# Kernel tuning notes

Measured on AMD Instinct MI355X. Metric: run time of the kernel, lower is better.

## Reference

```python
import jax, jax.numpy as jnp
import numpy as np

B, T_FRAMES, C, WS = 8, 8, 32, 128
N = 1024            # sample_size^2 points per frame
HW = WS * WS        # 16384 grid cells
BT = B * T_FRAMES


def setup_inputs() -> dict:
    key = jax.random.key(0)
    k1, k2, k3 = jax.random.split(key, 3)
    rng = np.random.default_rng(0)
    # per-frame grid-cell id for each of N points
    pose = rng.integers(0, HW, size=(BT, N))
    sorted_indices = np.argsort(pose, axis=1).astype(np.int32)
    sorted_pose = np.take_along_axis(pose, sorted_indices, axis=1)
    seq_unique_list = np.zeros((BT, N), dtype=np.int32)
    seq_unique_counts = np.zeros((BT, N), dtype=np.int32)
    for i in range(BT):
        u, c = np.unique(sorted_pose[i], return_counts=True)
        seq_unique_list[i, : len(u)] = u
        seq_unique_counts[i, : len(u)] = c
    return {
        "w_part": jax.random.normal(k1, (BT, N, C), dtype=jnp.float32),
        "sorted_indices": jnp.asarray(sorted_indices),
        "seq_unique_list": jnp.asarray(seq_unique_list),
        "seq_unique_counts": jnp.asarray(seq_unique_counts),
        "past_w": jax.random.normal(k2, (B, C, WS, WS), dtype=jnp.float32),
        "past_w_num_mask": jax.random.uniform(k3, (B, 1, WS, WS), dtype=jnp.float32) * 4.0,
        "T": T_FRAMES,
    }


def reference(w_part, sorted_indices, seq_unique_list, seq_unique_counts, past_w, past_w_num_mask, T):
    bt, n, c = w_part.shape
    b = bt // T
    ws = past_w.shape[2]
    hw = ws * ws
    # F.normalize(dim=-1), eps=1e-12
    wp = w_part / jnp.maximum(jnp.linalg.norm(w_part, axis=-1, keepdims=True), 1e-12)
    # gather: reorder points so same-cell points are contiguous
    gathered = jnp.take_along_axis(wp, sorted_indices[..., None].astype(jnp.int32), axis=1)  # (bt, n, c)
    counts = seq_unique_counts  # (bt, n) padded with zeros
    # segment id of each point from cumulative counts (points are sorted by cell)
    cum = jnp.cumsum(counts, axis=1)
    pt = jnp.arange(n)
    seg = jax.vmap(lambda cu: jnp.searchsorted(cu, pt, side='right'))(cum)  # (bt, n)
    sums = jax.vmap(lambda g, s: jax.ops.segment_sum(g, s, num_segments=n))(gathered, seg)  # (bt, n, c)
    means = sums / jnp.maximum(counts, 1)[..., None].astype(wp.dtype)
    # scatter means into dense grid; padded (count==0) slots routed out-of-bounds and dropped
    idx = jnp.where(counts > 0, seq_unique_list, hw)
    scat = jax.vmap(lambda m, i: jnp.zeros((hw, c), wp.dtype).at[i].set(m, mode='drop'))(means, idx)  # (bt, hw, c)
    mask = jax.vmap(lambda ct, i: jnp.zeros((hw,), wp.dtype).at[i].set(ct.astype(wp.dtype), mode='drop'))(counts, idx)
    new_w = scat.reshape(b, T, hw, c).mean(axis=1)                 # (b, hw, c)
    new_w = new_w.transpose(0, 2, 1).reshape(b, c, ws, ws)          # (b, c, ws, ws)
    w_num_mask = mask.reshape(b, T, hw).sum(axis=1).reshape(b, 1, ws, ws)
    # merge with past map; denominator is detached in the original
    new_w_num_mask = jax.lax.stop_gradient(w_num_mask) + jax.lax.stop_gradient(past_w_num_mask)
    new_w_num_mask = jnp.where(new_w_num_mask == 0, 1.0, new_w_num_mask)
    w = (new_w * w_num_mask + past_w * past_w_num_mask) / new_w_num_mask
    return w, new_w_num_mask
```

## Files before the change

### kernel.cpp

```cpp
#include <hip/hip_runtime.h>
#include <climits>

#define BATCH   8
#define TFRAMES 8
#define BT      (BATCH * TFRAMES)
#define NPTS    1024
#define NCH     32
#define WS      128
#define HW      (WS * WS)
#define CELLS   64
#define CHUNKS  (HW / CELLS)
#define CPAD    33
#define TPB     256

__global__ __launch_bounds__(256) void scan_kernel(
    const int* __restrict__ uniq_cnt,
    const int* __restrict__ uniq_list,
    int4*      __restrict__ entries,
    int*       __restrict__ ranges)
{
    __shared__ int s_key[NPTS];
    __shared__ int s_wsum[4];

    const int tid  = threadIdx.x;
    const int bt   = blockIdx.x;
    const int wave = tid >> 6;
    const int lane = tid & 63;

    const int4 c4 = reinterpret_cast<const int4*>(uniq_cnt + bt * NPTS)[tid];
    const int4 l4 = reinterpret_cast<const int4*>(uniq_list + bt * NPTS)[tid];
    s_key[tid * 4 + 0] = (c4.x > 0) ? l4.x : INT_MAX;
    s_key[tid * 4 + 1] = (c4.y > 0) ? l4.y : INT_MAX;
    s_key[tid * 4 + 2] = (c4.z > 0) ? l4.z : INT_MAX;
    s_key[tid * 4 + 3] = (c4.w > 0) ? l4.w : INT_MAX;

    const int lsum = c4.x + c4.y + c4.z + c4.w;

    int inc = lsum;
#pragma unroll
    for (int d = 1; d < 64; d <<= 1) {
        const int v = __shfl_up(inc, d);
        if (lane >= d) inc += v;
    }
    if (lane == 63) s_wsum[wave] = inc;
    __syncthreads();

    int woff = 0;
#pragma unroll
    for (int w = 0; w < 4; ++w)
        if (w < wave) woff += s_wsum[w];

    int st = woff + inc - lsum;
    int4* ep = entries + (size_t)bt * NPTS + tid * 4;
    ep[0] = make_int4(l4.x, c4.x, st, 0);             st += c4.x;
    ep[1] = make_int4(l4.y, c4.y, st, 0);             st += c4.y;
    ep[2] = make_int4(l4.z, c4.z, st, 0);             st += c4.z;
    ep[3] = make_int4(l4.w, c4.w, st, 0);

    for (int k = tid; k <= CHUNKS; k += 256) {
        const int X = k * CELLS;
        int lo = 0, hi = NPTS;
        while (lo < hi) {
            const int mid = (lo + hi) >> 1;
            if (s_key[mid] < X) lo = mid + 1; else hi = mid;
        }
        ranges[bt * (CHUNKS + 1) + k] = lo;
    }
}

__global__ __launch_bounds__(TPB, 8) void tile_kernel(
    const float* __restrict__ w_part,
    const int*   __restrict__ sorted_idx,
    const int4*  __restrict__ entries,
    const int*   __restrict__ ranges,
    const float* __restrict__ past_w,
    const float* __restrict__ past_mask,
    float*       __restrict__ out_w,
    float*       __restrict__ out_mask)
{
    __shared__ float s_acc[CELLS][CPAD];
    __shared__ float s_mask[CELLS];

    const int tid   = threadIdx.x;
    const int b     = blockIdx.x & (BATCH - 1);
    const int chunk = blockIdx.x >> 3;
    const int cb    = chunk * CELLS;

    const int cellq = tid & 15;
    const int cgrp  = tid >> 4;
    const int c0    = cgrp * 2;
    const int gc    = cb + cellq * 4;
    const size_t mbase = (size_t)b * HW + gc;
    const float4 pm4 = *reinterpret_cast<const float4*>(past_mask + mbase);
    const size_t a0 = ((size_t)b * NCH + c0) * HW + gc;
    const float4 pw0 = *reinterpret_cast<const float4*>(past_w + a0);
    const float4 pw1 = *reinterpret_cast<const float4*>(past_w + a0 + HW);

    float* flat = &s_acc[0][0];
    for (int i = tid; i < CELLS * CPAD; i += TPB) flat[i] = 0.0f;
    if (tid < CELLS) s_mask[tid] = 0.0f;
    __syncthreads();

    const int wave  = tid >> 6;
    const int lane  = tid & 63;
    const int slot  = lane >> 3;
    const int lane8 = lane & 7;

#pragma unroll
    for (int tt = 0; tt < 2; ++tt) {
        const int t  = wave * 2 + tt;
        const int bt = b * TFRAMES + t;
        const int lo = ranges[bt * (CHUNKS + 1) + chunk];
        const int hi = ranges[bt * (CHUNKS + 1) + chunk + 1];
        const int4* __restrict__ ent = entries + (size_t)bt * NPTS;
        const int*  __restrict__ si  = sorted_idx + bt * NPTS;
        const float* __restrict__ wp = w_part + (size_t)bt * NPTS * NCH;

        for (int e = lo + slot; e < hi; e += 8) {
            const int4 meta = ent[e];
            const int cell  = meta.x;
            const int cnt   = meta.y;
            const int start = meta.z;
            float4 lacc = make_float4(0.f, 0.f, 0.f, 0.f);
            for (int p = start; p < start + cnt; ++p) {
                const int j = si[p];
                const float4 v = *reinterpret_cast<const float4*>(
                    wp + (size_t)j * NCH + lane8 * 4);
                float ss = v.x * v.x + v.y * v.y + v.z * v.z + v.w * v.w;
                ss += __shfl_xor(ss, 1);
                ss += __shfl_xor(ss, 2);
                ss += __shfl_xor(ss, 4);
                const float scale = 1.0f / fmaxf(sqrtf(ss), 1e-12f);
                lacc.x += v.x * scale;
                lacc.y += v.y * scale;
                lacc.z += v.z * scale;
                lacc.w += v.w * scale;
            }
            const float invc = 1.0f / (float)cnt;
            const int cl = cell - cb;
            float* ap = &s_acc[cl][lane8 * 4];
            atomicAdd(ap + 0, lacc.x * invc);
            atomicAdd(ap + 1, lacc.y * invc);
            atomicAdd(ap + 2, lacc.z * invc);
            atomicAdd(ap + 3, lacc.w * invc);
            if (lane8 == 0) atomicAdd(&s_mask[cl], (float)cnt);
        }
    }
    __syncthreads();

    const float invT = 1.0f / (float)TFRAMES;
    float m[4], pm[4], r[4], dn[4];
    pm[0] = pm4.x; pm[1] = pm4.y; pm[2] = pm4.z; pm[3] = pm4.w;
#pragma unroll
    for (int i = 0; i < 4; ++i) {
        m[i] = s_mask[cellq * 4 + i];
        const float nwm = m[i] + pm[i];
        dn[i] = (nwm == 0.0f) ? 1.0f : nwm;
        r[i] = 1.0f / dn[i];
    }
    if (cgrp == 0) {
        *reinterpret_cast<float4*>(out_mask + mbase) =
            make_float4(dn[0], dn[1], dn[2], dn[3]);
    }

    float4 o0, o1;
    o0.x = (s_acc[cellq * 4 + 0][c0] * invT * m[0] + pw0.x * pm[0]) * r[0];
    o0.y = (s_acc[cellq * 4 + 1][c0] * invT * m[1] + pw0.y * pm[1]) * r[1];
    o0.z = (s_acc[cellq * 4 + 2][c0] * invT * m[2] + pw0.z * pm[2]) * r[2];
    o0.w = (s_acc[cellq * 4 + 3][c0] * invT * m[3] + pw0.w * pm[3]) * r[3];
    o1.x = (s_acc[cellq * 4 + 0][c0 + 1] * invT * m[0] + pw1.x * pm[0]) * r[0];
    o1.y = (s_acc[cellq * 4 + 1][c0 + 1] * invT * m[1] + pw1.y * pm[1]) * r[1];
    o1.z = (s_acc[cellq * 4 + 2][c0 + 1] * invT * m[2] + pw1.z * pm[2]) * r[2];
    o1.w = (s_acc[cellq * 4 + 3][c0 + 1] * invT * m[3] + pw1.w * pm[3]) * r[3];
    *reinterpret_cast<float4*>(out_w + a0)      = o0;
    *reinterpret_cast<float4*>(out_w + a0 + HW) = o1;
}

extern "C" void kernel_launch(void* const* d_in, const int* in_sizes, int n_in,
                              void* d_out, int out_size, void* d_ws, size_t ws_size,
                              hipStream_t stream) {
    (void)in_sizes; (void)n_in; (void)out_size; (void)ws_size;

    const float* w_part     = (const float*)d_in[0];
    const int*   sorted_idx = (const int*)d_in[1];
    const int*   uniq_list  = (const int*)d_in[2];
    const int*   uniq_cnt   = (const int*)d_in[3];
    const float* past_w     = (const float*)d_in[4];
    const float* past_mask  = (const float*)d_in[5];

    float* out      = (float*)d_out;
    float* out_w    = out;
    float* out_mask = out + (size_t)BATCH * NCH * HW;

    int4* entries = (int4*)d_ws;
    int*  ranges  = (int*)(entries + (size_t)BT * NPTS);

    scan_kernel<<<BT, 256, 0, stream>>>(uniq_cnt, uniq_list, entries, ranges);

    tile_kernel<<<BATCH * CHUNKS, TPB, 0, stream>>>(
        w_part, sorted_idx, entries, ranges,
        past_w, past_mask, out_w, out_mask);
}
```

Baseline: 29.86 us.

## Split segment-mean computation into separate point-parallel kernel before tile scatter

Adds a per-point segment-id map in the scan kernel and a new means_kernel that normalizes points in parallel and accumulates per-segment means via shared atomics, writing them to a workspace buffer. The tile kernel then reads precomputed means instead of looping serially over points per segment. This removes the variable-length inner loop and load imbalance from the tile kernel, at the cost of a memset, an extra kernel launch and a global round-trip of the means buffer.

```diff
diff --git a/kernel.cpp b/kernel.cpp
--- a/kernel.cpp
+++ b/kernel.cpp
@@ -17,9 +17,11 @@
     const int* __restrict__ uniq_cnt,
     const int* __restrict__ uniq_list,
     int4*      __restrict__ entries,
-    int*       __restrict__ ranges)
+    int*       __restrict__ ranges,
+    int*       __restrict__ segof)
 {
     __shared__ int s_key[NPTS];
+    __shared__ int s_segof[NPTS];
     __shared__ int s_wsum[4];
 
     const int tid  = threadIdx.x;
@@ -51,11 +53,25 @@
         if (w < wave) woff += s_wsum[w];
 
     int st = woff + inc - lsum;
-    int4* ep = entries + (size_t)bt * NPTS + tid * 4;
-    ep[0] = make_int4(l4.x, c4.x, st, 0);             st += c4.x;
-    ep[1] = make_int4(l4.y, c4.y, st, 0);             st += c4.y;
-    ep[2] = make_int4(l4.z, c4.z, st, 0);             st += c4.z;
+    const int e_base = tid * 4;
+    int4* ep = entries + (size_t)bt * NPTS + e_base;
+
+    ep[0] = make_int4(l4.x, c4.x, st, 0);
+    for (int q = 0; q < c4.x; ++q) s_segof[st + q] = e_base + 0;
+    st += c4.x;
+    ep[1] = make_int4(l4.y, c4.y, st, 0);
+    for (int q = 0; q < c4.y; ++q) s_segof[st + q] = e_base + 1;
+    st += c4.y;
+    ep[2] = make_int4(l4.z, c4.z, st, 0);
+    for (int q = 0; q < c4.z; ++q) s_segof[st + q] = e_base + 2;
+    st += c4.z;
     ep[3] = make_int4(l4.w, c4.w, st, 0);
+    for (int q = 0; q < c4.w; ++q) s_segof[st + q] = e_base + 3;
+
+    __syncthreads();
+
+    reinterpret_cast<int4*>(segof + bt * NPTS)[tid] =
+        *reinterpret_cast<int4*>(&s_segof[tid * 4]);
 
     for (int k = tid; k <= CHUNKS; k += 256) {
         const int X = k * CELLS;
@@ -68,9 +84,71 @@
     }
 }
 
-__global__ __launch_bounds__(TPB, 8) void tile_kernel(
+__global__ __launch_bounds__(256) void means_kernel(
     const float* __restrict__ w_part,
     const int*   __restrict__ sorted_idx,
+    const int*   __restrict__ segof,
+    const int4*  __restrict__ entries,
+    float*       __restrict__ means)
+{
+    __shared__ float s_seg[257][CPAD];
+
+    const int tid = threadIdx.x;
+    const int bt  = blockIdx.x >> 2;
+    const int p0  = (blockIdx.x & 3) * 256;
+
+    const int* __restrict__ sgo = segof + bt * NPTS;
+    const int s0 = sgo[p0];
+    const int s1 = sgo[p0 + 255];
+    const int nseg = s1 - s0 + 1;
+
+    float* flat = &s_seg[0][0];
+    for (int i = tid; i < nseg * CPAD; i += 256) flat[i] = 0.0f;
+    __syncthreads();
+
+    const int pt    = tid >> 3;
+    const int lane8 = tid & 7;
+    const int* __restrict__ si = sorted_idx + bt * NPTS;
+    const float* __restrict__ wp = w_part + (size_t)bt * NPTS * NCH;
+
+#pragma unroll
+    for (int pass = 0; pass < 8; ++pass) {
+        const int p = p0 + pass * 32 + pt;
+        const int j = si[p];
+        const float4 v = *reinterpret_cast<const float4*>(
+            wp + (size_t)j * NCH + lane8 * 4);
+        float ss = v.x * v.x + v.y * v.y + v.z * v.z + v.w * v.w;
+        ss += __shfl_xor(ss, 1);
+        ss += __shfl_xor(ss, 2);
+        ss += __shfl_xor(ss, 4);
+        const float scale = 1.0f / fmaxf(sqrtf(ss), 1e-12f);
+        const int ls = sgo[p] - s0;
+        float* ap = &s_seg[ls][lane8 * 4];
+        atomicAdd(ap + 0, v.x * scale);
+        atomicAdd(ap + 1, v.y * scale);
+        atomicAdd(ap + 2, v.z * scale);
+        atomicAdd(ap + 3, v.w * scale);
+    }
+    __syncthreads();
+
+    const int grp = tid >> 5;
+    const int ch  = tid & 31;
+    const int4* __restrict__ ent = entries + (size_t)bt * NPTS;
+    for (int le = grp; le < nseg; le += 8) {
+        const int e = s0 + le;
+        const int4 meta = ent[e];
+        const int cnt   = meta.y;
+        const int start = meta.z;
+        const float val = s_seg[le][ch] * (1.0f / (float)cnt);
+        float* dst = means + ((size_t)bt * NPTS + e) * NCH + ch;
+        const bool owned = (start >= p0) && (start + cnt <= p0 + 256);
+        if (owned) *dst = val;
+        else       atomicAdd(dst, val);
+    }
+}
+
+__global__ __launch_bounds__(TPB, 8) void tile_kernel(
+    const float* __restrict__ means,
     const int4*  __restrict__ entries,
     const int*   __restrict__ ranges,
     const float* __restrict__ past_w,
@@ -112,38 +190,20 @@
         const int bt = b * TFRAMES + t;
         const int lo = ranges[bt * (CHUNKS + 1) + chunk];
         const int hi = ranges[bt * (CHUNKS + 1) + chunk + 1];
-        const int4* __restrict__ ent = entries + (size_t)bt * NPTS;
-        const int*  __restrict__ si  = sorted_idx + bt * NPTS;
-        const float* __restrict__ wp = w_part + (size_t)bt * NPTS * NCH;
+        const int4*  __restrict__ ent = entries + (size_t)bt * NPTS;
+        const float* __restrict__ mns = means + (size_t)bt * NPTS * NCH;
 
         for (int e = lo + slot; e < hi; e += 8) {
             const int4 meta = ent[e];
-            const int cell  = meta.x;
-            const int cnt   = meta.y;
-            const int start = meta.z;
-            float4 lacc = make_float4(0.f, 0.f, 0.f, 0.f);
-            for (int p = start; p < start + cnt; ++p) {
-                const int j = si[p];
-                const float4 v = *reinterpret_cast<const float4*>(
-                    wp + (size_t)j * NCH + lane8 * 4);
-                float ss = v.x * v.x + v.y * v.y + v.z * v.z + v.w * v.w;
-                ss += __shfl_xor(ss, 1);
-                ss += __shfl_xor(ss, 2);
-                ss += __shfl_xor(ss, 4);
-                const float scale = 1.0f / fmaxf(sqrtf(ss), 1e-12f);
-                lacc.x += v.x * scale;
-                lacc.y += v.y * scale;
-                lacc.z += v.z * scale;
-                lacc.w += v.w * scale;
-            }
-            const float invc = 1.0f / (float)cnt;
-            const int cl = cell - cb;
+            const float4 mv = *reinterpret_cast<const float4*>(
+                mns + (size_t)e * NCH + lane8 * 4);
+            const int cl = meta.x - cb;
             float* ap = &s_acc[cl][lane8 * 4];
-            atomicAdd(ap + 0, lacc.x * invc);
-            atomicAdd(ap + 1, lacc.y * invc);
-            atomicAdd(ap + 2, lacc.z * invc);
-            atomicAdd(ap + 3, lacc.w * invc);
-            if (lane8 == 0) atomicAdd(&s_mask[cl], (float)cnt);
+            atomicAdd(ap + 0, mv.x);
+            atomicAdd(ap + 1, mv.y);
+            atomicAdd(ap + 2, mv.z);
+            atomicAdd(ap + 3, mv.w);
+            if (lane8 == 0) atomicAdd(&s_mask[cl], (float)meta.y);
         }
     }
     __syncthreads();
@@ -192,12 +252,17 @@
     float* out_w    = out;
     float* out_mask = out + (size_t)BATCH * NCH * HW;
 
-    int4* entries = (int4*)d_ws;
-    int*  ranges  = (int*)(entries + (size_t)BT * NPTS);
-
-    scan_kernel<<<BT, 256, 0, stream>>>(uniq_cnt, uniq_list, entries, ranges);
+    int4*  entries = (int4*)d_ws;
+    int*   ranges  = (int*)(entries + (size_t)BT * NPTS);
+    int*   segof   = ranges + (size_t)BT * (CHUNKS + 1);
+    float* means   = (float*)(segof + (size_t)BT * NPTS);
+
+    hipMemsetAsync(means, 0, (size_t)BT * NPTS * NCH * sizeof(float), stream);
+
+    scan_kernel<<<BT, 256, 0, stream>>>(uniq_cnt, uniq_list, entries, ranges, segof);
+
+    means_kernel<<<BT * 4, 256, 0, stream>>>(w_part, sorted_idx, segof, entries, means);
 
     tile_kernel<<<BATCH * CHUNKS, TPB, 0, stream>>>(
-        w_part, sorted_idx, entries, ranges,
-        past_w, past_mask, out_w, out_mask);
-}
+        means, entries, ranges, past_w, past_mask, out_w, out_mask);
+}
```

Result: slower. 62.73 us (+110.0%).

## Prefetch first point indices into entries and widen tiles to 128 cells

Applied to the files above, without the earlier changes.

The scan kernel now stores the first two sorted point indices of each cell directly in the entry record, packing the cell id and count together. It also writes (lo,hi) ranges as int2 pairs. The tile kernel doubles cells per block and threads per block, giving one wave per frame. It issues the metadata and first feature loads before zeroing shared memory, which shortens the dependent-load chain (entry, sorted index, feature). In exchange the scan kernel does extra gathers, and packing the count into the upper 16 bits assumes cell ids below 65536.

```diff
diff --git a/kernel.cpp b/kernel.cpp
--- a/kernel.cpp
+++ b/kernel.cpp
@@ -8,19 +8,21 @@
 #define NCH     32
 #define WS      128
 #define HW      (WS * WS)
-#define CELLS   64
+#define CELLS   128
 #define CHUNKS  (HW / CELLS)
 #define CPAD    33
-#define TPB     256
+#define TPB     512
 
 __global__ __launch_bounds__(256) void scan_kernel(
     const int* __restrict__ uniq_cnt,
     const int* __restrict__ uniq_list,
+    const int* __restrict__ sorted_idx,
     int4*      __restrict__ entries,
-    int*       __restrict__ ranges)
+    int2*      __restrict__ ranges2)
 {
     __shared__ int s_key[NPTS];
     __shared__ int s_wsum[4];
+    __shared__ int s_bnd[CHUNKS + 1];
 
     const int tid  = threadIdx.x;
     const int bt   = blockIdx.x;
@@ -50,29 +52,40 @@
     for (int w = 0; w < 4; ++w)
         if (w < wave) woff += s_wsum[w];
 
+    const int* __restrict__ si = sorted_idx + bt * NPTS;
     int st = woff + inc - lsum;
     int4* ep = entries + (size_t)bt * NPTS + tid * 4;
-    ep[0] = make_int4(l4.x, c4.x, st, 0);             st += c4.x;
-    ep[1] = make_int4(l4.y, c4.y, st, 0);             st += c4.y;
-    ep[2] = make_int4(l4.z, c4.z, st, 0);             st += c4.z;
-    ep[3] = make_int4(l4.w, c4.w, st, 0);
-
-    for (int k = tid; k <= CHUNKS; k += 256) {
-        const int X = k * CELLS;
+
+    const int cc[4] = {c4.x, c4.y, c4.z, c4.w};
+    const int ll[4] = {l4.x, l4.y, l4.z, l4.w};
+#pragma unroll
+    for (int k = 0; k < 4; ++k) {
+        const int cnt = cc[k];
+        const int j0  = (cnt > 0) ? si[st]     : 0;
+        const int j1  = (cnt > 1) ? si[st + 1] : 0;
+        ep[k] = make_int4(ll[k] | (cnt << 16), j0, j1, st);
+        st += cnt;
+    }
+
+    if (tid <= CHUNKS) {
+        const int X = tid * CELLS;
         int lo = 0, hi = NPTS;
         while (lo < hi) {
             const int mid = (lo + hi) >> 1;
             if (s_key[mid] < X) lo = mid + 1; else hi = mid;
         }
-        ranges[bt * (CHUNKS + 1) + k] = lo;
-    }
+        s_bnd[tid] = lo;
+    }
+    __syncthreads();
+    if (tid < CHUNKS)
+        ranges2[bt * CHUNKS + tid] = make_int2(s_bnd[tid], s_bnd[tid + 1]);
 }
 
 __global__ __launch_bounds__(TPB, 8) void tile_kernel(
     const float* __restrict__ w_part,
     const int*   __restrict__ sorted_idx,
     const int4*  __restrict__ entries,
-    const int*   __restrict__ ranges,
+    const int2*  __restrict__ ranges2,
     const float* __restrict__ past_w,
     const float* __restrict__ past_mask,
     float*       __restrict__ out_w,
@@ -86,8 +99,8 @@
     const int chunk = blockIdx.x >> 3;
     const int cb    = chunk * CELLS;
 
-    const int cellq = tid & 15;
-    const int cgrp  = tid >> 4;
+    const int cellq = tid & 31;
+    const int cgrp  = tid >> 5;
     const int c0    = cgrp * 2;
     const int gc    = cb + cellq * 4;
     const size_t mbase = (size_t)b * HW + gc;
@@ -96,55 +109,84 @@
     const float4 pw0 = *reinterpret_cast<const float4*>(past_w + a0);
     const float4 pw1 = *reinterpret_cast<const float4*>(past_w + a0 + HW);
 
-    float* flat = &s_acc[0][0];
-    for (int i = tid; i < CELLS * CPAD; i += TPB) flat[i] = 0.0f;
-    if (tid < CELLS) s_mask[tid] = 0.0f;
-    __syncthreads();
-
     const int wave  = tid >> 6;
     const int lane  = tid & 63;
     const int slot  = lane >> 3;
     const int lane8 = lane & 7;
 
-#pragma unroll
-    for (int tt = 0; tt < 2; ++tt) {
-        const int t  = wave * 2 + tt;
-        const int bt = b * TFRAMES + t;
-        const int lo = ranges[bt * (CHUNKS + 1) + chunk];
-        const int hi = ranges[bt * (CHUNKS + 1) + chunk + 1];
-        const int4* __restrict__ ent = entries + (size_t)bt * NPTS;
-        const int*  __restrict__ si  = sorted_idx + bt * NPTS;
-        const float* __restrict__ wp = w_part + (size_t)bt * NPTS * NCH;
-
-        for (int e = lo + slot; e < hi; e += 8) {
-            const int4 meta = ent[e];
-            const int cell  = meta.x;
-            const int cnt   = meta.y;
-            const int start = meta.z;
-            float4 lacc = make_float4(0.f, 0.f, 0.f, 0.f);
-            for (int p = start; p < start + cnt; ++p) {
+    const int bt = b * TFRAMES + wave;
+    const int2 rg = ranges2[bt * CHUNKS + chunk];
+    const int lo = rg.x, hi = rg.y;
+
+    const int4* __restrict__ ent = entries + (size_t)bt * NPTS;
+    const float* __restrict__ wp = w_part + (size_t)bt * NPTS * NCH;
+
+    const int eA = lo + slot;
+    const int eB = eA + 8;
+    const bool vA = (eA < hi);
+    const bool vB = (eB < hi);
+    const int4 metaA = ent[vA ? eA : 0];
+    const int4 metaB = ent[vB ? eB : 0];
+    const float4 vwA = *reinterpret_cast<const float4*>(
+        wp + (size_t)metaA.y * NCH + lane8 * 4);
+    const float4 vwB = *reinterpret_cast<const float4*>(
+        wp + (size_t)metaB.y * NCH + lane8 * 4);
+
+    float* flat = &s_acc[0][0];
+    for (int i = tid; i < CELLS * CPAD; i += TPB) flat[i] = 0.0f;
+    if (tid < CELLS) s_mask[tid] = 0.0f;
+    __syncthreads();
+
+    const int* __restrict__ si = sorted_idx + bt * NPTS;
+    auto process = [&](const int4 meta, const float4 v0) {
+        const int cell  = meta.x & 0xFFFF;
+        const int cnt   = meta.x >> 16;
+        float ss = v0.x * v0.x + v0.y * v0.y + v0.z * v0.z + v0.w * v0.w;
+        ss += __shfl_xor(ss, 1);
+        ss += __shfl_xor(ss, 2);
+        ss += __shfl_xor(ss, 4);
+        const float s0 = 1.0f / fmaxf(sqrtf(ss), 1e-12f);
+        float4 lacc = make_float4(v0.x * s0, v0.y * s0, v0.z * s0, v0.w * s0);
+        if (cnt > 1) {
+            const float4 v1 = *reinterpret_cast<const float4*>(
+                wp + (size_t)meta.z * NCH + lane8 * 4);
+            float s1 = v1.x * v1.x + v1.y * v1.y + v1.z * v1.z + v1.w * v1.w;
+            s1 += __shfl_xor(s1, 1);
+            s1 += __shfl_xor(s1, 2);
+            s1 += __shfl_xor(s1, 4);
+            s1 = 1.0f / fmaxf(sqrtf(s1), 1e-12f);
+            lacc.x += v1.x * s1; lacc.y += v1.y * s1;
+            lacc.z += v1.z * s1; lacc.w += v1.w * s1;
+            for (int p = meta.w + 2; p < meta.w + cnt; ++p) {
                 const int j = si[p];
                 const float4 v = *reinterpret_cast<const float4*>(
                     wp + (size_t)j * NCH + lane8 * 4);
-                float ss = v.x * v.x + v.y * v.y + v.z * v.z + v.w * v.w;
-                ss += __shfl_xor(ss, 1);
-                ss += __shfl_xor(ss, 2);
-                ss += __shfl_xor(ss, 4);
-                const float scale = 1.0f / fmaxf(sqrtf(ss), 1e-12f);
-                lacc.x += v.x * scale;
-                lacc.y += v.y * scale;
-                lacc.z += v.z * scale;
-                lacc.w += v.w * scale;
+                float sv = v.x * v.x + v.y * v.y + v.z * v.z + v.w * v.w;
+                sv += __shfl_xor(sv, 1);
+                sv += __shfl_xor(sv, 2);
+                sv += __shfl_xor(sv, 4);
+                sv = 1.0f / fmaxf(sqrtf(sv), 1e-12f);
+                lacc.x += v.x * sv; lacc.y += v.y * sv;
+                lacc.z += v.z * sv; lacc.w += v.w * sv;
             }
-            const float invc = 1.0f / (float)cnt;
-            const int cl = cell - cb;
-            float* ap = &s_acc[cl][lane8 * 4];
-            atomicAdd(ap + 0, lacc.x * invc);
-            atomicAdd(ap + 1, lacc.y * invc);
-            atomicAdd(ap + 2, lacc.z * invc);
-            atomicAdd(ap + 3, lacc.w * invc);
-            if (lane8 == 0) atomicAdd(&s_mask[cl], (float)cnt);
         }
+        const float invc = 1.0f / (float)cnt;
+        const int cl = cell - cb;
+        float* ap = &s_acc[cl][lane8 * 4];
+        atomicAdd(ap + 0, lacc.x * invc);
+        atomicAdd(ap + 1, lacc.y * invc);
+        atomicAdd(ap + 2, lacc.z * invc);
+        atomicAdd(ap + 3, lacc.w * invc);
+        if (lane8 == 0) atomicAdd(&s_mask[cl], (float)cnt);
+    };
+
+    if (vA) process(metaA, vwA);
+    if (vB) process(metaB, vwB);
+    for (int e = lo + 16 + slot; e < hi; e += 8) {
+        const int4 meta = ent[e];
+        const float4 v0 = *reinterpret_cast<const float4*>(
+            wp + (size_t)meta.y * NCH + lane8 * 4);
+        process(meta, v0);
     }
     __syncthreads();
 
@@ -193,11 +235,12 @@
     float* out_mask = out + (size_t)BATCH * NCH * HW;
 
     int4* entries = (int4*)d_ws;
-    int*  ranges  = (int*)(entries + (size_t)BT * NPTS);
-
-    scan_kernel<<<BT, 256, 0, stream>>>(uniq_cnt, uniq_list, entries, ranges);
+    int2* ranges2 = (int2*)(entries + (size_t)BT * NPTS);
+
+    scan_kernel<<<BT, 256, 0, stream>>>(uniq_cnt, uniq_list, sorted_idx,
+                                        entries, ranges2);
 
     tile_kernel<<<BATCH * CHUNKS, TPB, 0, stream>>>(
-        w_part, sorted_idx, entries, ranges,
+        w_part, sorted_idx, entries, ranges2,
         past_w, past_mask, out_w, out_mask);
 }
```

Result: no change. 29.62 us (-0.8%).

## Replace cell-chunk gather with per-point global atomic scatter and separate combine

Applied to the files above, without the earlier changes.

The scan kernel now writes a packed (cell, count) per original point index instead of segment entries and chunk ranges. A new points kernel has each point normalize itself and atomically add its scaled vector and a unit count into a zeroed global accumulator. A combine kernel then merges that accumulator with the past map. This removes the per-segment serial loop and the binary searches, at the cost of a memset of the full accumulator, an extra launch, and many global float atomics.

```diff
diff --git a/kernel.cpp b/kernel.cpp
--- a/kernel.cpp
+++ b/kernel.cpp
@@ -1,5 +1,4 @@
 #include <hip/hip_runtime.h>
-#include <climits>
 
 #define BATCH   8
 #define TFRAMES 8
@@ -8,18 +7,16 @@
 #define NCH     32
 #define WS      128
 #define HW      (WS * WS)
-#define CELLS   64
+#define CELLS   128
 #define CHUNKS  (HW / CELLS)
 #define CPAD    33
-#define TPB     256
 
 __global__ __launch_bounds__(256) void scan_kernel(
     const int* __restrict__ uniq_cnt,
     const int* __restrict__ uniq_list,
-    int4*      __restrict__ entries,
-    int*       __restrict__ ranges)
+    const int* __restrict__ sorted_idx,
+    int*       __restrict__ cellcnt)
 {
-    __shared__ int s_key[NPTS];
     __shared__ int s_wsum[4];
 
     const int tid  = threadIdx.x;
@@ -29,11 +26,6 @@
 
     const int4 c4 = reinterpret_cast<const int4*>(uniq_cnt + bt * NPTS)[tid];
     const int4 l4 = reinterpret_cast<const int4*>(uniq_list + bt * NPTS)[tid];
-    s_key[tid * 4 + 0] = (c4.x > 0) ? l4.x : INT_MAX;
-    s_key[tid * 4 + 1] = (c4.y > 0) ? l4.y : INT_MAX;
-    s_key[tid * 4 + 2] = (c4.z > 0) ? l4.z : INT_MAX;
-    s_key[tid * 4 + 3] = (c4.w > 0) ? l4.w : INT_MAX;
-
     const int lsum = c4.x + c4.y + c4.z + c4.w;
 
     int inc = lsum;
@@ -51,129 +43,130 @@
         if (w < wave) woff += s_wsum[w];
 
     int st = woff + inc - lsum;
-    int4* ep = entries + (size_t)bt * NPTS + tid * 4;
-    ep[0] = make_int4(l4.x, c4.x, st, 0);             st += c4.x;
-    ep[1] = make_int4(l4.y, c4.y, st, 0);             st += c4.y;
-    ep[2] = make_int4(l4.z, c4.z, st, 0);             st += c4.z;
-    ep[3] = make_int4(l4.w, c4.w, st, 0);
-
-    for (int k = tid; k <= CHUNKS; k += 256) {
-        const int X = k * CELLS;
-        int lo = 0, hi = NPTS;
-        while (lo < hi) {
-            const int mid = (lo + hi) >> 1;
-            if (s_key[mid] < X) lo = mid + 1; else hi = mid;
-        }
-        ranges[bt * (CHUNKS + 1) + k] = lo;
-    }
-}
-
-__global__ __launch_bounds__(TPB, 8) void tile_kernel(
+    const int* __restrict__ si = sorted_idx + bt * NPTS;
+    int* __restrict__ cco = cellcnt + bt * NPTS;
+
+    const int cc[4] = {c4.x, c4.y, c4.z, c4.w};
+    const int ll[4] = {l4.x, l4.y, l4.z, l4.w};
+#pragma unroll
+    for (int k = 0; k < 4; ++k) {
+        const int cnt  = cc[k];
+        const int pack = ll[k] | (cnt << 16);
+        for (int q = 0; q < cnt; ++q)
+            cco[si[st + q]] = pack;
+        st += cnt;
+    }
+}
+
+__global__ __launch_bounds__(256) void points_kernel(
     const float* __restrict__ w_part,
-    const int*   __restrict__ sorted_idx,
-    const int4*  __restrict__ entries,
-    const int*   __restrict__ ranges,
+    const int*   __restrict__ cellcnt,
+    float*       __restrict__ acc,
+    float*       __restrict__ mask)
+{
+    const int tid  = threadIdx.x;
+    const int b    = blockIdx.x & (BATCH - 1);
+    const int rest = blockIdx.x >> 3;
+    const int t    = rest >> 5;
+    const int j0   = (rest & 31) * 32;
+    const int bt   = b * TFRAMES + t;
+
+    const int pt    = tid >> 3;
+    const int lane8 = tid & 7;
+    const int j     = j0 + pt;
+
+    const float4 v = *reinterpret_cast<const float4*>(
+        w_part + ((size_t)bt * NPTS + j) * NCH + lane8 * 4);
+    float ss = v.x * v.x + v.y * v.y + v.z * v.z + v.w * v.w;
+    ss += __shfl_xor(ss, 1);
+    ss += __shfl_xor(ss, 2);
+    ss += __shfl_xor(ss, 4);
+
+    const int cc   = cellcnt[bt * NPTS + j];
+    const int cell = cc & 0xFFFF;
+    const int cnt  = cc >> 16;
+    const float sc = 1.0f / (fmaxf(sqrtf(ss), 1e-12f) * (float)cnt);
+
+    float* ap = acc + ((size_t)b * HW + cell) * NCH + lane8 * 4;
+    atomicAdd(ap + 0, v.x * sc);
+    atomicAdd(ap + 1, v.y * sc);
+    atomicAdd(ap + 2, v.z * sc);
+    atomicAdd(ap + 3, v.w * sc);
+    if (lane8 == 0) atomicAdd(mask + (size_t)b * HW + cell, 1.0f);
+}
+
+__global__ __launch_bounds__(256) void combine_kernel(
+    const float* __restrict__ acc,
+    const float* __restrict__ maskacc,
     const float* __restrict__ past_w,
     const float* __restrict__ past_mask,
     float*       __restrict__ out_w,
     float*       __restrict__ out_mask)
 {
-    __shared__ float s_acc[CELLS][CPAD];
-    __shared__ float s_mask[CELLS];
+    __shared__ float s[CELLS][CPAD];
 
     const int tid   = threadIdx.x;
     const int b     = blockIdx.x & (BATCH - 1);
     const int chunk = blockIdx.x >> 3;
     const int cb    = chunk * CELLS;
 
-    const int cellq = tid & 15;
-    const int cgrp  = tid >> 4;
-    const int c0    = cgrp * 2;
-    const int gc    = cb + cellq * 4;
-    const size_t mbase = (size_t)b * HW + gc;
-    const float4 pm4 = *reinterpret_cast<const float4*>(past_mask + mbase);
-    const size_t a0 = ((size_t)b * NCH + c0) * HW + gc;
-    const float4 pw0 = *reinterpret_cast<const float4*>(past_w + a0);
-    const float4 pw1 = *reinterpret_cast<const float4*>(past_w + a0 + HW);
-
-    float* flat = &s_acc[0][0];
-    for (int i = tid; i < CELLS * CPAD; i += TPB) flat[i] = 0.0f;
-    if (tid < CELLS) s_mask[tid] = 0.0f;
-    __syncthreads();
-
-    const int wave  = tid >> 6;
-    const int lane  = tid & 63;
-    const int slot  = lane >> 3;
-    const int lane8 = lane & 7;
-
-#pragma unroll
-    for (int tt = 0; tt < 2; ++tt) {
-        const int t  = wave * 2 + tt;
-        const int bt = b * TFRAMES + t;
-        const int lo = ranges[bt * (CHUNKS + 1) + chunk];
-        const int hi = ranges[bt * (CHUNKS + 1) + chunk + 1];
-        const int4* __restrict__ ent = entries + (size_t)bt * NPTS;
-        const int*  __restrict__ si  = sorted_idx + bt * NPTS;
-        const float* __restrict__ wp = w_part + (size_t)bt * NPTS * NCH;
-
-        for (int e = lo + slot; e < hi; e += 8) {
-            const int4 meta = ent[e];
-            const int cell  = meta.x;
-            const int cnt   = meta.y;
-            const int start = meta.z;
-            float4 lacc = make_float4(0.f, 0.f, 0.f, 0.f);
-            for (int p = start; p < start + cnt; ++p) {
-                const int j = si[p];
-                const float4 v = *reinterpret_cast<const float4*>(
-                    wp + (size_t)j * NCH + lane8 * 4);
-                float ss = v.x * v.x + v.y * v.y + v.z * v.z + v.w * v.w;
-                ss += __shfl_xor(ss, 1);
-                ss += __shfl_xor(ss, 2);
-                ss += __shfl_xor(ss, 4);
-                const float scale = 1.0f / fmaxf(sqrtf(ss), 1e-12f);
-                lacc.x += v.x * scale;
-                lacc.y += v.y * scale;
-                lacc.z += v.z * scale;
-                lacc.w += v.w * scale;
-            }
-            const float invc = 1.0f / (float)cnt;
-            const int cl = cell - cb;
-            float* ap = &s_acc[cl][lane8 * 4];
-            atomicAdd(ap + 0, lacc.x * invc);
-            atomicAdd(ap + 1, lacc.y * invc);
-            atomicAdd(ap + 2, lacc.z * invc);
-            atomicAdd(ap + 3, lacc.w * invc);
-            if (lane8 == 0) atomicAdd(&s_mask[cl], (float)cnt);
-        }
-    }
-    __syncthreads();
-
+    const int cellq = tid & 31;
+    const int cgrp  = tid >> 5;
+    const int c0    = cgrp * 4;
     const float invT = 1.0f / (float)TFRAMES;
-    float m[4], pm[4], r[4], dn[4];
-    pm[0] = pm4.x; pm[1] = pm4.y; pm[2] = pm4.z; pm[3] = pm4.w;
+
+    float m[4], pm[4], dn[4], r[4];
 #pragma unroll
     for (int i = 0; i < 4; ++i) {
-        m[i] = s_mask[cellq * 4 + i];
+        const int gcell = cb + cellq + 32 * i;
+        m[i]  = maskacc [(size_t)b * HW + gcell];
+        pm[i] = past_mask[(size_t)b * HW + gcell];
+    }
+    float pw[4][4];
+#pragma unroll
+    for (int c = 0; c < 4; ++c)
+#pragma unroll
+        for (int i = 0; i < 4; ++i)
+            pw[c][i] = past_w[((size_t)b * NCH + c0 + c) * HW + cb + cellq + 32 * i];
+
+    const float4* ab = reinterpret_cast<const float4*>(
+        acc + ((size_t)b * HW + cb) * NCH);
+#pragma unroll
+    for (int k = 0; k < 4; ++k) {
+        const int idx = tid + k * 256;
+        const float4 f = ab[idx];
+        const int cell = idx >> 3;
+        const int ch   = (idx & 7) * 4;
+        s[cell][ch + 0] = f.x;
+        s[cell][ch + 1] = f.y;
+        s[cell][ch + 2] = f.z;
+        s[cell][ch + 3] = f.w;
+    }
+
+#pragma unroll
+    for (int i = 0; i < 4; ++i) {
         const float nwm = m[i] + pm[i];
         dn[i] = (nwm == 0.0f) ? 1.0f : nwm;
-        r[i] = 1.0f / dn[i];
-    }
+        r[i]  = 1.0f / dn[i];
+    }
+    __syncthreads();
+
     if (cgrp == 0) {
-        *reinterpret_cast<float4*>(out_mask + mbase) =
-            make_float4(dn[0], dn[1], dn[2], dn[3]);
-    }
-
-    float4 o0, o1;
-    o0.x = (s_acc[cellq * 4 + 0][c0] * invT * m[0] + pw0.x * pm[0]) * r[0];
-    o0.y = (s_acc[cellq * 4 + 1][c0] * invT * m[1] + pw0.y * pm[1]) * r[1];
-    o0.z = (s_acc[cellq * 4 + 2][c0] * invT * m[2] + pw0.z * pm[2]) * r[2];
-    o0.w = (s_acc[cellq * 4 + 3][c0] * invT * m[3] + pw0.w * pm[3]) * r[3];
-    o1.x = (s_acc[cellq * 4 + 0][c0 + 1] * invT * m[0] + pw1.x * pm[0]) * r[0];
-    o1.y = (s_acc[cellq * 4 + 1][c0 + 1] * invT * m[1] + pw1.y * pm[1]) * r[1];
-    o1.z = (s_acc[cellq * 4 + 2][c0 + 1] * invT * m[2] + pw1.z * pm[2]) * r[2];
-    o1.w = (s_acc[cellq * 4 + 3][c0 + 1] * invT * m[3] + pw1.w * pm[3]) * r[3];
-    *reinterpret_cast<float4*>(out_w + a0)      = o0;
-    *reinterpret_cast<float4*>(out_w + a0 + HW) = o1;
+#pragma unroll
+        for (int i = 0; i < 4; ++i)
+            out_mask[(size_t)b * HW + cb + cellq + 32 * i] = dn[i];
+    }
+
+#pragma unroll
+    for (int c = 0; c < 4; ++c) {
+#pragma unroll
+        for (int i = 0; i < 4; ++i) {
+            const int cell = cellq + 32 * i;
+            const float nw = s[cell][c0 + c] * invT;
+            out_w[((size_t)b * NCH + c0 + c) * HW + cb + cell] =
+                (nw * m[i] + pw[c][i] * pm[i]) * r[i];
+        }
+    }
 }
 
 extern "C" void kernel_launch(void* const* d_in, const int* in_sizes, int n_in,
@@ -192,12 +185,17 @@
     float* out_w    = out;
     float* out_mask = out + (size_t)BATCH * NCH * HW;
 
-    int4* entries = (int4*)d_ws;
-    int*  ranges  = (int*)(entries + (size_t)BT * NPTS);
-
-    scan_kernel<<<BT, 256, 0, stream>>>(uniq_cnt, uniq_list, entries, ranges);
-
-    tile_kernel<<<BATCH * CHUNKS, TPB, 0, stream>>>(
-        w_part, sorted_idx, entries, ranges,
-        past_w, past_mask, out_w, out_mask);
-}
+    float* acc     = (float*)d_ws;
+    float* maskacc = acc + (size_t)BATCH * HW * NCH;
+    int*   cellcnt = (int*)(maskacc + (size_t)BATCH * HW);
+
+    hipMemsetAsync(acc, 0,
+                   (size_t)BATCH * HW * (NCH + 1) * sizeof(float), stream);
+
+    scan_kernel<<<BT, 256, 0, stream>>>(uniq_cnt, uniq_list, sorted_idx, cellcnt);
+
+    points_kernel<<<BT * 32, 256, 0, stream>>>(w_part, cellcnt, acc, maskacc);
+
+    combine_kernel<<<BATCH * CHUNKS, 256, 0, stream>>>(
+        acc, maskacc, past_w, past_mask, out_w, out_mask);
+}
```

Result: slower. 63.69 us (+113.3%).
